# Performance work log

Hardware: AMD Instinct MI355X
Metric: run time of the kernel (lower is better)

Reference implementation:

```python
import jax, jax.numpy as jnp
import numpy as np

B, L, N, C = 16, 96, 1024, 3
EMB, GRAP, OUT, NLAYER = 64, 16, 12, 2


def setup_inputs() -> dict:
    key = jax.random.key(0)
    ks = jax.random.split(key, 16)
    s = 0.1
    return {
        "history_data": jax.random.normal(ks[0], (B, L, N, C), jnp.float32),
        # row-stochastic graph (normalized adjacency buffer)
        "adj": jax.nn.softmax(jax.random.normal(ks[1], (N, N), jnp.float32), axis=-1),
        "Wv0": jax.random.normal(ks[2], (C, EMB), jnp.float32) * s,
        "Wv1": jax.random.normal(ks[3], (EMB, EMB), jnp.float32) * s,
        "bv": jnp.zeros((NLAYER, EMB), jnp.float32),
        "E": jax.random.normal(ks[4], (NLAYER, N, EMB), jnp.float32) * s,
        "Wq": jax.random.normal(ks[5], (NLAYER, EMB, EMB), jnp.float32) * s,
        "Wk": jax.random.normal(ks[6], (NLAYER, EMB, EMB), jnp.float32) * s,
        "Eg1": jax.random.normal(ks[7], (NLAYER, N, GRAP), jnp.float32) * s,
        "Eg2": jax.random.normal(ks[8], (NLAYER, N, GRAP), jnp.float32) * s,
        "Wmix": jax.random.normal(ks[9], (NLAYER, 3, EMB, EMB), jnp.float32) * s,
        "bmix": jnp.zeros((NLAYER, EMB), jnp.float32),
        "Wgates": jax.random.normal(ks[10], (NLAYER, 4, EMB, EMB), jnp.float32) * s,
        "bgates": jnp.zeros((NLAYER, 4, EMB), jnp.float32),
        "Wdec": jax.random.normal(ks[11], (OUT, NLAYER, EMB), jnp.float32) * s,
        "bdec": jnp.zeros((OUT,), jnp.float32),
        "Wout": jax.random.normal(ks[12], (OUT, OUT), jnp.float32) * s,
        "bout": jnp.zeros((OUT,), jnp.float32),
    }


def reference(history_data, adj, Wv0, Wv1, bv, E, Wq, Wk, Eg1, Eg2,
              Wmix, bmix, Wgates, bgates, Wdec, bdec, Wout, bout):
    # GinAR forward (inference: dropout = identity, lay_norm unused in original forward).
    emb = Wv1.shape[0]
    inv = 1.0 / jnp.sqrt(jnp.float32(emb))
    x = history_data  # (B, L, N, in)
    finals = []
    for z in range(Wmix.shape[0]):
        Wv = Wv0 if z == 0 else Wv1
        # interpolation attention over variables (nodes), shared across time/batch
        q = E[z] @ Wq[z]
        k = E[z] @ Wk[z]
        attn = jax.nn.softmax((q @ k.T) * inv, axis=-1)                 # (N, N)
        # adaptive learned graph
        adp = jax.nn.softmax(jax.nn.relu(Eg1[z] @ Eg2[z].T), axis=-1)    # (N, N)
        bz, Wm, bm, Wg, bgz = bv[z], Wmix[z], bmix[z], Wgates[z], bgates[z]

        def step(ct, xt, Wv=Wv, attn=attn, adp=adp, bz=bz, Wm=Wm, bm=bm, Wg=Wg, bgz=bgz):
            v = xt @ Wv + bz                                # (B, N, emb)
            h = jnp.einsum('mn,bne->bme', attn, v)          # variable interpolation
            hg = (jnp.einsum('mn,bne->bme', adj, h) @ Wm[0]
                  + jnp.einsum('mn,bne->bme', adp, h) @ Wm[1]
                  + h @ Wm[2] + bm)                         # adaptive graph conv
            gates = jnp.einsum('bne,kef->kbnf', hg, Wg) + bgz[:, None, None, :]
            f = jax.nn.sigmoid(gates[0])
            i = jax.nn.sigmoid(gates[1])
            g = jnp.tanh(gates[2])
            o = jax.nn.sigmoid(gates[3])
            ct = f * ct + i * g
            ht = o * jnp.tanh(ct)
            return ct, ht

        ct0 = jnp.zeros((x.shape[0], x.shape[2], emb), x.dtype)
        _, hts = jax.lax.scan(step, ct0, jnp.moveaxis(x, 1, 0))  # (L, B, N, emb)
        x = jnp.moveaxis(hts, 0, 1)                              # (B, L, N, emb)
        finals.append(x[:, -1])                                  # last step -> (B, N, emb)
    final = jnp.stack(finals, axis=1)                            # (B, layers, N, emb)
    # decoder Conv2d(layer_num -> out_len, kernel (1, emb)) == contraction over (layer, emb)
    dec = jnp.einsum('blne,ole->bon', final, Wdec) + bdec[None, :, None]
    # 1x1 output conv
    out = jnp.einsum('bpn,op->bon', dec, Wout) + bout[None, :, None]
    return out  # (B, out_len, N)
```

## Files before the change

### kernel.cpp

```cpp
#include <hip/hip_runtime.h>
#include <hip/hip_bf16.h>

#define B_ 16
#define L_ 96
#define N_ 1024
#define EMB_ 64

typedef __hip_bfloat16 bf16;
typedef __attribute__((ext_vector_type(4))) float f32x4;
typedef __attribute__((ext_vector_type(8))) short s16x8;

template <int MODE>
__global__ __launch_bounds__(256) void gemm_nn(
    const float* __restrict__ A, const float* __restrict__ Bm, float* __restrict__ C,
    int M, int N, int K, int lda, int ldb, int ldc, const float* __restrict__ bias)
{
    if (MODE == 1) {
        const int bz = blockIdx.z, z = bz >> 1;
        A += (size_t)z * 65536;
        const float* Wsel = (bz & 1) ? (const float*)bias : Bm;
        Bm = Wsel + z * 4096;
        C += (size_t)bz * 65536;
        bias = nullptr;
    }
    __shared__ float As[64][17];
    __shared__ __align__(16) float Bs[16][64];
    const int tid = threadIdx.x;
    const int tx = tid & 15, ty = tid >> 4;
    const int row0 = blockIdx.y * 64, col0 = blockIdx.x * 64;
    float acc[4][4] = {};
    const int ak = tid & 15, ar = tid >> 4;
    const int bc = tid & 63, bk = tid >> 6;
    for (int k0 = 0; k0 < K; k0 += 16) {
#pragma unroll
        for (int i = 0; i < 4; ++i) {
            int r = ar + i * 16;
            int gr = row0 + r, gk = k0 + ak;
            As[r][ak] = (gr < M && gk < K) ? A[(size_t)gr * lda + gk] : 0.f;
        }
#pragma unroll
        for (int i = 0; i < 4; ++i) {
            int kk = bk + i * 4;
            int gk = k0 + kk, gc = col0 + bc;
            Bs[kk][bc] = (gk < K && gc < N) ? Bm[(size_t)gk * ldb + gc] : 0.f;
        }
        __syncthreads();
#pragma unroll
        for (int kk = 0; kk < 16; ++kk) {
            float4 b4 = *reinterpret_cast<const float4*>(&Bs[kk][tx * 4]);
            float a0 = As[ty * 4 + 0][kk];
            float a1 = As[ty * 4 + 1][kk];
            float a2 = As[ty * 4 + 2][kk];
            float a3 = As[ty * 4 + 3][kk];
            acc[0][0] += a0 * b4.x; acc[0][1] += a0 * b4.y; acc[0][2] += a0 * b4.z; acc[0][3] += a0 * b4.w;
            acc[1][0] += a1 * b4.x; acc[1][1] += a1 * b4.y; acc[1][2] += a1 * b4.z; acc[1][3] += a1 * b4.w;
            acc[2][0] += a2 * b4.x; acc[2][1] += a2 * b4.y; acc[2][2] += a2 * b4.z; acc[2][3] += a2 * b4.w;
            acc[3][0] += a3 * b4.x; acc[3][1] += a3 * b4.y; acc[3][2] += a3 * b4.z; acc[3][3] += a3 * b4.w;
        }
        __syncthreads();
    }
#pragma unroll
    for (int i = 0; i < 4; ++i) {
        int gr = row0 + ty * 4 + i;
        if (gr >= M) continue;
#pragma unroll
        for (int j = 0; j < 4; ++j) {
            int gc = col0 + tx * 4 + j;
            if (gc >= N) continue;
            float v = acc[i][j];
            if (bias) v += bias[gc];
            C[(size_t)gr * ldc + gc] = v;
        }
    }
}

__global__ __launch_bounds__(256) void gemm_nt(
    const float* __restrict__ A, const float* __restrict__ Bm, float* __restrict__ C,
    int N, int K, float alpha, int zsA, int zsB, int zsC)
{
    const int z = blockIdx.z;
    A += (size_t)z * zsA; Bm += (size_t)z * zsB; C += (size_t)z * zsC;
    __shared__ float As[64][65];
    __shared__ float Bs[64][65];
    const int tid = threadIdx.x;
    const int row0 = blockIdx.y * 64, col0 = blockIdx.x * 64;
    for (int idx = tid; idx < 64 * K; idx += 256) {
        int r = idx / K, c = idx % K;
        As[r][c] = A[(size_t)(row0 + r) * K + c];
        Bs[r][c] = Bm[(size_t)(col0 + r) * K + c];
    }
    __syncthreads();
    const int tx = tid & 15, ty = tid >> 4;
    float acc[4][4] = {};
    for (int c = 0; c < K; ++c) {
        float a[4], b[4];
#pragma unroll
        for (int i = 0; i < 4; ++i) a[i] = As[ty * 4 + i][c];
#pragma unroll
        for (int j = 0; j < 4; ++j) b[j] = Bs[tx * 4 + j][c];
#pragma unroll
        for (int i = 0; i < 4; ++i)
#pragma unroll
            for (int j = 0; j < 4; ++j) acc[i][j] += a[i] * b[j];
    }
#pragma unroll
    for (int i = 0; i < 4; ++i)
#pragma unroll
        for (int j = 0; j < 4; ++j)
            C[(size_t)(row0 + ty * 4 + i) * N + col0 + tx * 4 + j] = alpha * acc[i][j];
}

__global__ __launch_bounds__(256) void row_softmax(
    const float* __restrict__ in, float* __restrict__ out32, int os32,
    bf16* __restrict__ out16, int os16, int zs_in, int zs16, int relu)
{
    const int z = blockIdx.y;
    const float* rp = in + (size_t)z * zs_in + (size_t)blockIdx.x * N_;
    if (out32) out32 += (size_t)z * zs_in;
    if (out16) out16 += (size_t)z * zs16;
    const int tid = threadIdx.x;
    float v[4];
#pragma unroll
    for (int j = 0; j < 4; ++j) {
        float x = rp[tid + 256 * j];
        if (relu) x = fmaxf(x, 0.f);
        v[j] = x;
    }
    float m = fmaxf(fmaxf(v[0], v[1]), fmaxf(v[2], v[3]));
#pragma unroll
    for (int off = 32; off > 0; off >>= 1) m = fmaxf(m, __shfl_xor(m, off));
    __shared__ float red[4], red2[4];
    int w = tid >> 6;
    if ((tid & 63) == 0) red[w] = m;
    __syncthreads();
    m = fmaxf(fmaxf(red[0], red[1]), fmaxf(red[2], red[3]));
    float s = 0.f;
#pragma unroll
    for (int j = 0; j < 4; ++j) { v[j] = __expf(v[j] - m); s += v[j]; }
#pragma unroll
    for (int off = 32; off > 0; off >>= 1) s += __shfl_xor(s, off);
    if ((tid & 63) == 0) red2[w] = s;
    __syncthreads();
    s = red2[0] + red2[1] + red2[2] + red2[3];
    float inv = 1.f / s;
#pragma unroll
    for (int j = 0; j < 4; ++j) {
        float r = v[j] * inv;
        if (out32) out32[(size_t)blockIdx.x * os32 + tid + 256 * j] = r;
        if (out16) out16[(size_t)blockIdx.x * os16 + tid + 256 * j] = __float2bfloat16(r);
    }
}

__global__ __launch_bounds__(256) void transpose_f2b(
    const float* __restrict__ in, bf16* __restrict__ out)
{
    const int z = blockIdx.z;
    in += (size_t)z * 1048576; out += (size_t)z * 1048576;
    __shared__ float t[64][65];
    const int cx = blockIdx.x, cy = blockIdx.y;
    const int tid = threadIdx.x;
#pragma unroll
    for (int k = 0; k < 16; ++k) {
        int idx = k * 256 + tid;
        int r = idx >> 6, c = idx & 63;
        t[r][c] = in[(size_t)(cy * 64 + r) * 1024 + cx * 64 + c];
    }
    __syncthreads();
#pragma unroll
    for (int k = 0; k < 16; ++k) {
        int idx = k * 256 + tid;
        int r = idx >> 6, c = idx & 63;
        out[(size_t)(cx * 64 + r) * 1024 + cy * 64 + c] = __float2bfloat16(t[c][r]);
    }
}

__global__ __launch_bounds__(256) void wgct_kernel(const float* __restrict__ Wg,
                                                   bf16* __restrict__ WgcT)
{
    int i = blockIdx.x * 256 + threadIdx.x;
    int g = i >> 12, e = (i >> 6) & 63, f = i & 63;
    WgcT[(((size_t)g * 64 + f) << 6) + e] = __float2bfloat16(Wg[i]);
}

__global__ __launch_bounds__(256) void wvc1t_kernel(const float* __restrict__ Wvc1,
                                                    bf16* __restrict__ WT)
{
    int i = blockIdx.x * 256 + threadIdx.x;
    int row = i >> 6, f = i & 63;
    float v = 0.f;
    if (row < 192) { int kp = row >> 6, e = row & 63; v = Wvc1[kp * 4096 + f * 64 + e]; }
    WT[i] = __float2bfloat16(v);
}

__global__ __launch_bounds__(256) void f2b_kernel(const float* __restrict__ in,
                                                  bf16* __restrict__ out, int n)
{
    int i = blockIdx.x * 256 + threadIdx.x;
    if (i < n) out[i] = __float2bfloat16(in[i]);
}

__global__ __launch_bounds__(256) void bias_kernel(
    const float* __restrict__ bvz, const float* __restrict__ Wmz, const float* __restrict__ bmz,
    const float* __restrict__ Wgz, const float* __restrict__ bgz, float* __restrict__ bgconst)
{
    __shared__ float bconst[64];
    const int tid = threadIdx.x;
    if (tid < 64) {
        float s = bmz[tid];
        for (int kp = 0; kp < 3; ++kp)
            for (int f = 0; f < 64; ++f) s += bvz[f] * Wmz[kp * 4096 + f * 64 + tid];
        bconst[tid] = s;
    }
    __syncthreads();
    int g = tid >> 6, fo = tid & 63;
    float s = bgz[g * 64 + fo];
    for (int e = 0; e < 64; ++e) s += bconst[e] * Wgz[g * 4096 + e * 64 + fo];
    bgconst[tid] = s;
}

__global__ __launch_bounds__(256) void wbig_kernel(
    const float* __restrict__ Wvc0, const float* __restrict__ Wg0, bf16* __restrict__ WbigT)
{
    const int tid = threadIdx.x;
    const int g = tid >> 6, fo = tid & 63;
    float v[9];
#pragma unroll
    for (int q = 0; q < 9; ++q) {
        const int kp = q / 3, c = q % 3;
        float s = 0.f;
        for (int e = 0; e < 64; ++e)
            s += Wvc0[kp * 192 + c * 64 + e] * Wg0[g * 4096 + e * 64 + fo];
        v[q] = s;
    }
#pragma unroll
    for (int i = 0; i < 32; ++i)
        WbigT[(size_t)tid * 32 + i] = __float2bfloat16(i < 9 ? v[i] : 0.f);
}

__global__ __launch_bounds__(256) void xt_build(
    const float* __restrict__ hist, bf16* __restrict__ XT)
{
    __shared__ float xs[3][1024];
    const int lb = blockIdx.x;
    const int l = lb >> 4, b = lb & 15;
    const int tid = threadIdx.x;
    const float* xp = hist + ((size_t)b * L_ + l) * N_ * 3;
    for (int i = tid; i < 3072; i += 256) xs[i % 3][i / 3] = xp[i];
    __syncthreads();
#pragma unroll
    for (int c = 0; c < 3; ++c)
#pragma unroll
        for (int q = 0; q < 4; ++q) {
            int n = q * 256 + tid;
            XT[((size_t)lb * 3 + c) * 1024 + n] = __float2bfloat16(xs[c][n]);
        }
}

__device__ __forceinline__ void gload16(const bf16* g, bf16* l)
{
    __builtin_amdgcn_global_load_lds((const __attribute__((address_space(1))) void*)g,
                                     (__attribute__((address_space(3))) void*)l, 16, 0, 0);
}

template <int OUT_BF16, int REMAP>
__global__ __launch_bounds__(256) void gemm_mfma(
    const bf16* __restrict__ A, const bf16* __restrict__ BT, void* __restrict__ Cp,
    int M, int N, int K, int lda, int ldb, int ldc,
    const float* __restrict__ bias, int Nmask)
{
    __shared__ __align__(16) bf16 As[128 * 64];
    __shared__ __align__(16) bf16 Bs[128 * 64];
    const int tid = threadIdx.x;
    const int lane = tid & 63, w = tid >> 6;
    const int wr = w >> 1, wc = w & 1;
    const int row0 = blockIdx.y * 128, col0 = blockIdx.x * 128;
    if (REMAP == 1) BT += (size_t)blockIdx.z * 64;
    if (REMAP == 2) A += (size_t)blockIdx.z * 1024;
    if (REMAP == 3) {
        const int z3 = blockIdx.z >> 1, wh = blockIdx.z & 1;
        if (wh) A = BT + (size_t)z3 * 1048576;
        BT = (const bf16*)bias + (size_t)z3 * 1048576;
        Cp = (void*)((bf16*)Cp + (size_t)z3 * 3145728 + (size_t)wh * 1024);
        bias = nullptr;
    }

    f32x4 acc[4][4];
#pragma unroll
    for (int i = 0; i < 4; ++i)
#pragma unroll
        for (int j = 0; j < 4; ++j) acc[i][j] = (f32x4){0.f, 0.f, 0.f, 0.f};

    const int srow = w * 32 + (lane >> 3);
    const int scolsw = ((lane & 7) ^ (lane >> 3)) * 8;

    for (int k0 = 0; k0 < K; k0 += 64) {
#pragma unroll
        for (int i = 0; i < 4; ++i) {
            gload16(A + (size_t)(row0 + srow + i * 8) * lda + k0 + scolsw,
                    &As[(w * 32 + i * 8) * 64]);
            gload16(BT + (size_t)(col0 + srow + i * 8) * ldb + k0 + scolsw,
                    &Bs[(w * 32 + i * 8) * 64]);
        }
        __syncthreads();
#pragma unroll
        for (int kk = 0; kk < 64; kk += 32) {
            s16x8 af[4], bfr[4];
            const int ko = (kk + (lane >> 4) * 8) ^ ((lane & 7) << 3);
#pragma unroll
            for (int mi = 0; mi < 4; ++mi)
                af[mi] = *(const s16x8*)&As[(wr * 64 + mi * 16 + (lane & 15)) * 64 + ko];
#pragma unroll
            for (int ni = 0; ni < 4; ++ni)
                bfr[ni] = *(const s16x8*)&Bs[(wc * 64 + ni * 16 + (lane & 15)) * 64 + ko];
#pragma unroll
            for (int mi = 0; mi < 4; ++mi)
#pragma unroll
                for (int ni = 0; ni < 4; ++ni)
                    acc[mi][ni] = __builtin_amdgcn_mfma_f32_16x16x32_bf16(
                        af[mi], bfr[ni], acc[mi][ni], 0, 0, 0);
        }
        __syncthreads();
    }

    if (REMAP == 1) {
        bf16* outb = (bf16*)Cp + (size_t)blockIdx.z * (64 * 3072);
#pragma unroll
        for (int mi = 0; mi < 4; ++mi) {
            const int gr = row0 + wr * 64 + mi * 16 + (lane >> 4) * 4;
#pragma unroll
            for (int ni = 0; ni < 4; ++ni) {
                const int gc = col0 + wc * 64 + ni * 16 + (lane & 15);
#pragma unroll
                for (int j = 0; j < 4; ++j) {
                    const int r = gr + j;
                    if (r >= Nmask) continue;
                    outb[(size_t)(r & 63) * 3072 + (r >> 6) * 1024 + gc] =
                        __float2bfloat16(acc[mi][ni][j]);
                }
            }
        }
        return;
    }
    if (REMAP == 2) {
        bf16* outb = (bf16*)Cp;
        const int kpoff = blockIdx.z * 3;
#pragma unroll
        for (int mi = 0; mi < 4; ++mi) {
            const int gr = row0 + wr * 64 + mi * 16 + (lane >> 4) * 4;
#pragma unroll
            for (int ni = 0; ni < 4; ++ni) {
                const int gc = col0 + wc * 64 + ni * 16 + (lane & 15);
                if (gc >= Nmask) continue;
                const int dstc = (gc / 3) * 32 + kpoff + gc % 3;
#pragma unroll
                for (int j = 0; j < 4; ++j)
                    outb[(size_t)(gr + j) * ldc + dstc] = __float2bfloat16(acc[mi][ni][j]);
            }
        }
        return;
    }

#pragma unroll
    for (int mi = 0; mi < 4; ++mi) {
        const int gr = row0 + wr * 64 + mi * 16 + (lane >> 4) * 4;
#pragma unroll
        for (int ni = 0; ni < 4; ++ni) {
            const int gc = col0 + wc * 64 + ni * 16 + (lane & 15);
            if (gc >= Nmask) continue;
            const float bb = bias ? bias[gc] : 0.f;
#pragma unroll
            for (int j = 0; j < 4; ++j) {
                float v = acc[mi][ni][j] + bb;
                if (OUT_BF16)
                    ((bf16*)Cp)[(size_t)(gr + j) * ldc + gc] = __float2bfloat16(v);
                else
                    ((float*)Cp)[(size_t)(gr + j) * ldc + gc] = v;
            }
        }
    }
}

__global__ __launch_bounds__(512) void gemm_pipe(
    const bf16* __restrict__ A, const bf16* __restrict__ BT, bf16* __restrict__ C,
    int N, int K)
{
    __shared__ __align__(16) bf16 lds[8 * 8192];
    const int tid = threadIdx.x;
    const int lane = tid & 63, w = tid >> 6;
    const int wm = w >> 2, wn = w & 3, bh = wn >> 1;
    const int row0 = blockIdx.y * 256, col0 = blockIdx.x * 256;

    const int strow = tid >> 3;
    const int srck  = ((tid & 7) ^ ((tid >> 3) & 7)) << 3;
    const int e7 = lane & 7, fs = lane >> 4, a15 = lane & 15;

    int aoff0[8], boff0[4];
#pragma unroll
    for (int mi = 0; mi < 8; ++mi)
        aoff0[mi] = (mi * 16 + a15) * 64 + ((fs ^ e7) << 3);
#pragma unroll
    for (int ni = 0; ni < 4; ++ni)
        boff0[ni] = ((wn & 1) * 64 + ni * 16 + a15) * 64 + ((fs ^ e7) << 3);

    auto stage = [&](int mat, int half, int kt) {
        bf16* dst = &lds[(size_t)((((kt & 1) << 1) | mat) * 2 + half) * 8192 + w * 512];
        const bf16* src = (mat ? BT + (size_t)col0 * K : A + (size_t)row0 * K)
                          + (size_t)(half * 128) * K + kt * 64 + srck;
        gload16(src + (size_t)strow * K, dst);
        gload16(src + (size_t)(64 + strow) * K, dst + 4096);
    };

    f32x4 acc[8][4];
#pragma unroll
    for (int i = 0; i < 8; ++i)
#pragma unroll
        for (int j = 0; j < 4; ++j) acc[i][j] = (f32x4){0.f, 0.f, 0.f, 0.f};

    s16x8 b0, b1, b2, b3;

#define MF_(a, mi) { \
    acc[mi][0] = __builtin_amdgcn_mfma_f32_16x16x32_bf16(a, b0, acc[mi][0], 0, 0, 0); \
    acc[mi][1] = __builtin_amdgcn_mfma_f32_16x16x32_bf16(a, b1, acc[mi][1], 0, 0, 0); \
    acc[mi][2] = __builtin_amdgcn_mfma_f32_16x16x32_bf16(a, b2, acc[mi][2], 0, 0, 0); \
    acc[mi][3] = __builtin_amdgcn_mfma_f32_16x16x32_bf16(a, b3, acc[mi][3], 0, 0, 0); }

#define PH_(d, kh, g, DOB, STG) { \
    const bf16* Ab = &lds[((d) * 4 + wm) * 8192]; \
    const bf16* Bb = &lds[((d) * 4 + 2 + bh) * 8192]; \
    if (DOB) { \
        b0 = *(const s16x8*)&Bb[boff0[0] ^ ((kh) * 32)]; \
        b1 = *(const s16x8*)&Bb[boff0[1] ^ ((kh) * 32)]; \
        b2 = *(const s16x8*)&Bb[boff0[2] ^ ((kh) * 32)]; \
        b3 = *(const s16x8*)&Bb[boff0[3] ^ ((kh) * 32)]; \
    } \
    s16x8 a0 = *(const s16x8*)&Ab[aoff0[(g) * 4 + 0] ^ ((kh) * 32)]; \
    s16x8 a1 = *(const s16x8*)&Ab[aoff0[(g) * 4 + 1] ^ ((kh) * 32)]; \
    s16x8 a2 = *(const s16x8*)&Ab[aoff0[(g) * 4 + 2] ^ ((kh) * 32)]; \
    s16x8 a3 = *(const s16x8*)&Ab[aoff0[(g) * 4 + 3] ^ ((kh) * 32)]; \
    STG; \
    __builtin_amdgcn_s_barrier(); \
    asm volatile("s_waitcnt lgkmcnt(0)" ::: "memory"); \
    __builtin_amdgcn_sched_barrier(0); \
    __builtin_amdgcn_s_setprio(1); \
    MF_(a0, (g) * 4 + 0); MF_(a1, (g) * 4 + 1); \
    MF_(a2, (g) * 4 + 2); MF_(a3, (g) * 4 + 3); \
    __builtin_amdgcn_s_setprio(0); \
    __builtin_amdgcn_s_barrier(); }

    const int NT = K >> 6;
    stage(0, 0, 0); stage(0, 1, 0); stage(1, 0, 0); stage(1, 1, 0);
    stage(0, 0, 1);

    for (int i = 0; i < NT / 2; ++i) {
        const int kt = 2 * i;
        asm volatile("s_waitcnt vmcnt(2)" ::: "memory");
        __builtin_amdgcn_sched_barrier(0);
        __builtin_amdgcn_s_barrier();
        PH_(0, 0, 0, 1, { stage(0, 1, kt + 1); });
        PH_(0, 0, 1, 0, { stage(1, 0, kt + 1); });
        PH_(0, 1, 0, 1, { stage(1, 1, kt + 1); });
        PH_(0, 1, 1, 0, { if (kt + 2 < NT) stage(0, 0, kt + 2); });
        if (kt + 2 < NT) { asm volatile("s_waitcnt vmcnt(2)" ::: "memory"); }
        else             { asm volatile("s_waitcnt vmcnt(0)" ::: "memory"); }
        __builtin_amdgcn_sched_barrier(0);
        __builtin_amdgcn_s_barrier();
        PH_(1, 0, 0, 1, { if (kt + 2 < NT) stage(0, 1, kt + 2); });
        PH_(1, 0, 1, 0, { if (kt + 2 < NT) stage(1, 0, kt + 2); });
        PH_(1, 1, 0, 1, { if (kt + 2 < NT) stage(1, 1, kt + 2); });
        PH_(1, 1, 1, 0, { if (kt + 3 < NT) stage(0, 0, kt + 3); });
    }
#undef PH_
#undef MF_

#pragma unroll
    for (int mi = 0; mi < 8; ++mi) {
        const int gr = row0 + wm * 128 + mi * 16 + (lane >> 4) * 4;
#pragma unroll
        for (int ni = 0; ni < 4; ++ni) {
            const int gc = col0 + wn * 64 + ni * 16 + (lane & 15);
#pragma unroll
            for (int j = 0; j < 4; ++j)
                C[(size_t)(gr + j) * N + gc] = __float2bfloat16(acc[mi][ni][j]);
        }
    }
}

__global__ __launch_bounds__(256, 4) void fused_gates_scan(
    const bf16* __restrict__ HG, const bf16* __restrict__ WgcT,
    const float* __restrict__ bgc, float* __restrict__ ct_buf,
    bf16* __restrict__ ht_out, float* __restrict__ htlast,
    int LC, int l0, int initct)
{
    __shared__ __align__(16) bf16 Bs[256 * 64];
    __shared__ float bgs[256];
    const int tid = threadIdx.x;
    const int lane = tid & 63, w = tid >> 6;
    const int n = blockIdx.x;
    const int swz = ((lane & 7) ^ (lane >> 3)) * 8;
    const int l8 = (lane >> 3) * 64;

#pragma unroll
    for (int r = 0; r < 8; ++r)
        gload16(WgcT + r * 2048 + w * 512 + l8 + swz, &Bs[r * 2048 + w * 512]);
    bgs[tid] = bgc[tid];
    __syncthreads();

    const int ar = lane & 15;
    const int ak = (lane >> 4) * 8;
    const int kswz = (lane & 7) << 3;
    const int f = w * 16 + ar;
    const int r0 = (lane >> 4) * 4;
    const float bgf = bgs[f], bgi = bgs[64 + f], bgg = bgs[128 + f], bgo = bgs[192 + f];

    float ct[4];
    const size_t cbase = (size_t)n * 1024;
#pragma unroll
    for (int j = 0; j < 4; ++j)
        ct[j] = initct ? 0.f : ct_buf[cbase + (size_t)(r0 + j) * 64 + f];

    const bf16* HGn = HG + (size_t)n * LC * 1024;
    s16x8 a0 = *(const s16x8*)&HGn[ar * 64 + ak];
    s16x8 a1 = *(const s16x8*)&HGn[ar * 64 + ak + 32];

    for (int l = 0; l < LC; ++l) {
        s16x8 p0 = a0, p1 = a1;
        if (l + 1 < LC) {
            p0 = *(const s16x8*)&HGn[((l + 1) * 16 + ar) * 64 + ak];
            p1 = *(const s16x8*)&HGn[((l + 1) * 16 + ar) * 64 + ak + 32];
        }
        f32x4 acc[4];
#pragma unroll
        for (int ni = 0; ni < 4; ++ni) acc[ni] = (f32x4){0.f, 0.f, 0.f, 0.f};
#pragma unroll
        for (int ni = 0; ni < 4; ++ni) {
            s16x8 bf = *(const s16x8*)&Bs[(ni * 64 + w * 16 + ar) * 64 + (ak ^ kswz)];
            acc[ni] = __builtin_amdgcn_mfma_f32_16x16x32_bf16(a0, bf, acc[ni], 0, 0, 0);
        }
#pragma unroll
        for (int ni = 0; ni < 4; ++ni) {
            s16x8 bf = *(const s16x8*)&Bs[(ni * 64 + w * 16 + ar) * 64 + ((ak + 32) ^ kswz)];
            acc[ni] = __builtin_amdgcn_mfma_f32_16x16x32_bf16(a1, bf, acc[ni], 0, 0, 0);
        }
        const size_t hbase = ((size_t)n * LC + l) * 1024;
        const bool last = (l0 + l == L_ - 1);
#pragma unroll
        for (int j = 0; j < 4; ++j) {
            float xf = acc[0][j] + bgf;
            float xi = acc[1][j] + bgi;
            float xg = acc[2][j] + bgg;
            float xo = acc[3][j] + bgo;
            float fg = 1.f / (1.f + __expf(-xf));
            float ig = 1.f / (1.f + __expf(-xi));
            float gg = 2.f / (1.f + __expf(-2.f * xg)) - 1.f;
            float og = 1.f / (1.f + __expf(-xo));
            ct[j] = fg * ct[j] + ig * gg;
            float ht = og * (2.f / (1.f + __expf(-2.f * ct[j])) - 1.f);
            if (ht_out) ht_out[hbase + (size_t)(r0 + j) * 64 + f] = __float2bfloat16(ht);
            if (htlast && last) htlast[cbase + (size_t)(r0 + j) * 64 + f] = ht;
        }
        a0 = p0; a1 = p1;
    }
#pragma unroll
    for (int j = 0; j < 4; ++j)
        ct_buf[cbase + (size_t)(r0 + j) * 64 + f] = ct[j];
}

__global__ __launch_bounds__(256, 4) void fused_gates_scan_y(
    const bf16* __restrict__ Y, const bf16* __restrict__ WbigT,
    const float* __restrict__ bgc, float* __restrict__ ct_buf,
    bf16* __restrict__ ht_out, float* __restrict__ htlast,
    int LC, int l0, int initct)
{
    __shared__ bf16 Bs2[256 * 40];
    __shared__ float bgs[256];
    const int tid = threadIdx.x;
    const int lane = tid & 63, w = tid >> 6;
    const int n = blockIdx.x;
    {
        const uint4* src = (const uint4*)(WbigT + (size_t)tid * 32);
        uint4* dst = (uint4*)&Bs2[tid * 40];
        dst[0] = src[0]; dst[1] = src[1]; dst[2] = src[2]; dst[3] = src[3];
    }
    bgs[tid] = bgc[tid];
    __syncthreads();

    const int ar = lane & 15, fs = lane >> 4;
    const int f = w * 16 + ar;
    const int r0 = fs * 4;
    const float bgf = bgs[f], bgi = bgs[64 + f], bgg = bgs[128 + f], bgo = bgs[192 + f];

    float ct[4];
    const size_t cbase = (size_t)n * 1024;
#pragma unroll
    for (int j = 0; j < 4; ++j)
        ct[j] = initct ? 0.f : ct_buf[cbase + (size_t)(r0 + j) * 64 + f];

    const bf16* Yn = Y + (size_t)n * LC * 512;
    s16x8 a = *(const s16x8*)&Yn[ar * 32 + fs * 8];

    for (int l = 0; l < LC; ++l) {
        s16x8 p = a;
        if (l + 1 < LC) p = *(const s16x8*)&Yn[((l + 1) * 16 + ar) * 32 + fs * 8];
        f32x4 acc[4];
#pragma unroll
        for (int ni = 0; ni < 4; ++ni) {
            s16x8 bf = *(const s16x8*)&Bs2[(ni * 64 + w * 16 + ar) * 40 + fs * 8];
            acc[ni] = __builtin_amdgcn_mfma_f32_16x16x32_bf16(
                a, bf, (f32x4){0.f, 0.f, 0.f, 0.f}, 0, 0, 0);
        }
        const size_t hbase = ((size_t)n * LC + l) * 1024;
        const bool last = (l0 + l == L_ - 1);
#pragma unroll
        for (int j = 0; j < 4; ++j) {
            float xf = acc[0][j] + bgf;
            float xi = acc[1][j] + bgi;
            float xg = acc[2][j] + bgg;
            float xo = acc[3][j] + bgo;
            float fg = 1.f / (1.f + __expf(-xf));
            float ig = 1.f / (1.f + __expf(-xi));
            float gg = 2.f / (1.f + __expf(-2.f * xg)) - 1.f;
            float og = 1.f / (1.f + __expf(-xo));
            ct[j] = fg * ct[j] + ig * gg;
            float ht = og * (2.f / (1.f + __expf(-2.f * ct[j])) - 1.f);
            if (ht_out) ht_out[hbase + (size_t)(r0 + j) * 64 + f] = __float2bfloat16(ht);
            if (htlast && last) htlast[cbase + (size_t)(r0 + j) * 64 + f] = ht;
        }
        a = p;
    }
#pragma unroll
    for (int j = 0; j < 4; ++j)
        ct_buf[cbase + (size_t)(r0 + j) * 64 + f] = ct[j];
}

__global__ __launch_bounds__(256) void decoder_kernel(
    const float* __restrict__ h0, const float* __restrict__ h1,
    const float* __restrict__ Wdec, const float* __restrict__ bdec,
    const float* __restrict__ Wout, const float* __restrict__ bout,
    float* __restrict__ outp)
{
    __shared__ float Wd[12 * 2 * 64];
    __shared__ float Wo[144];
    __shared__ float bd[12], bo[12];
    const int tid = threadIdx.x;
    for (int i = tid; i < 12 * 2 * 64; i += 256) Wd[i] = Wdec[i];
    for (int i = tid; i < 144; i += 256) Wo[i] = Wout[i];
    if (tid < 12) { bd[tid] = bdec[tid]; bo[tid] = bout[tid]; }
    __syncthreads();
    const int gid = blockIdx.x * 256 + tid;
    const int b = gid >> 10, n = gid & 1023;
    const float* h0r = h0 + ((size_t)n * 16 + b) * 64;
    const float* h1r = h1 + ((size_t)n * 16 + b) * 64;
    float dec[12];
#pragma unroll
    for (int o = 0; o < 12; ++o) dec[o] = bd[o];
    for (int e = 0; e < 64; ++e) {
        float v0 = h0r[e], v1 = h1r[e];
#pragma unroll
        for (int o = 0; o < 12; ++o) dec[o] += v0 * Wd[o * 128 + e] + v1 * Wd[o * 128 + 64 + e];
    }
#pragma unroll
    for (int o = 0; o < 12; ++o) {
        float s = bo[o];
#pragma unroll
        for (int p = 0; p < 12; ++p) s += Wo[o * 12 + p] * dec[p];
        outp[((size_t)b * 12 + o) * 1024 + n] = s;
    }
}

extern "C" void kernel_launch(void* const* d_in, const int* in_sizes, int n_in,
                              void* d_out, int out_size, void* d_ws, size_t ws_size,
                              hipStream_t stream)
{
    const float* hist = (const float*)d_in[0];
    const float* adj  = (const float*)d_in[1];
    const float* Wv0  = (const float*)d_in[2];
    const float* Wv1  = (const float*)d_in[3];
    const float* bv   = (const float*)d_in[4];
    const float* E    = (const float*)d_in[5];
    const float* Wq   = (const float*)d_in[6];
    const float* Wk   = (const float*)d_in[7];
    const float* Eg1  = (const float*)d_in[8];
    const float* Eg2  = (const float*)d_in[9];
    const float* Wmix = (const float*)d_in[10];
    const float* bmix = (const float*)d_in[11];
    const float* Wg   = (const float*)d_in[12];
    const float* bg   = (const float*)d_in[13];
    const float* Wdec = (const float*)d_in[14];
    const float* bdec = (const float*)d_in[15];
    const float* Wout = (const float*)d_in[16];
    const float* bout = (const float*)d_in[17];
    float* outp = (float*)d_out;
    (void)in_sizes; (void)n_in; (void)out_size;

    char* ws = (char*)d_ws;
    size_t off = 0;
    auto alloc = [&](size_t bytes) -> void* {
        void* p = (void*)(ws + off);
        off += (bytes + 255) & ~(size_t)255;
        return p;
    };
    bf16*  Mcatb  = (bf16*)alloc((size_t)2 * 1024 * 3072 * 2);
    bf16*  attnT2 = (bf16*)alloc((size_t)2 * 1024 * 1024 * 2);
    bf16*  adjb   = (bf16*)alloc((size_t)1024 * 1024 * 2);
    bf16*  adpb2  = (bf16*)alloc((size_t)2 * 1024 * 1024 * 2);
    float* qkb    = (float*)alloc((size_t)4 * 1024 * 64 * 4);
    float* logit2 = (float*)alloc((size_t)2 * 1024 * 1024 * 4);
    float* Wvc0   = (float*)alloc(3 * 3 * 64 * 4);
    float* Wvc1   = (float*)alloc(3 * 64 * 64 * 4);
    bf16*  Wvc1T  = (bf16*)alloc(256 * 64 * 2);
    bf16*  WgcT1  = (bf16*)alloc(256 * 64 * 2);
    bf16*  WbigT  = (bf16*)alloc(256 * 32 * 2);
    float* bgc0   = (float*)alloc(256 * 4);
    float* bgc1   = (float*)alloc(256 * 4);
    float* ct0    = (float*)alloc((size_t)N_ * B_ * 64 * 4);
    float* ct1    = (float*)alloc((size_t)N_ * B_ * 64 * 4);
    float* hl0    = (float*)alloc((size_t)N_ * B_ * 64 * 4);
    float* hl1    = (float*)alloc((size_t)N_ * B_ * 64 * 4);
    bf16*  XT     = (bf16*)alloc((size_t)L_ * 16 * 3 * 1024 * 2);
    size_t fixed = off;

    static const int divs[] = {16, 8};
    int LC = 8;
    for (int di = 0; di < 2; ++di) {
        if (fixed + (size_t)divs[di] * 9437184ull + 65536 <= ws_size) { LC = divs[di]; break; }
    }
    bf16*  VcatT = (bf16*)alloc((size_t)LC * 6291456ull);
    bf16*  HGht  = (bf16*)alloc((size_t)LC * 2097152ull);
    bf16*  Y     = (bf16*)alloc((size_t)LC * 1048576ull);

    dim3 blk(256);
    bf16*  McatB[2] = {Mcatb, Mcatb + 3145728};
    float* bgc[2] = {bgc0, bgc1};

    f2b_kernel<<<4096, blk, 0, stream>>>(adj, adjb, 1024 * 1024);
    gemm_nn<1><<<dim3(1, 16, 4), blk, 0, stream>>>(E, Wq, qkb,
        1024, 64, 64, 64, 64, 64, (const float*)Wk);
    gemm_nt<<<dim3(16, 16, 2), blk, 0, stream>>>(qkb, qkb + 65536, logit2,
        1024, 64, 0.125f, 131072, 131072, 1048576);
    row_softmax<<<dim3(1024, 2), blk, 0, stream>>>(logit2, logit2, 1024,
        Mcatb + 2048, 3072, 1048576, 3145728, 0);
    transpose_f2b<<<dim3(16, 16, 2), blk, 0, stream>>>(logit2, attnT2);
    gemm_nt<<<dim3(16, 16, 2), blk, 0, stream>>>(Eg1, Eg2, logit2,
        1024, 16, 1.f, 16384, 16384, 1048576);
    row_softmax<<<dim3(1024, 2), blk, 0, stream>>>(logit2, nullptr, 0,
        adpb2, 1024, 1048576, 1048576, 1);
    for (int kp = 0; kp < 3; ++kp)
        gemm_nn<0><<<dim3(1, 1), blk, 0, stream>>>(Wv0, Wmix + kp * 4096,
            Wvc0 + kp * 3 * 64, 3, 64, 64, 64, 64, 64, nullptr);
    wbig_kernel<<<1, blk, 0, stream>>>(Wvc0, Wg, WbigT);
    for (int kp = 0; kp < 3; ++kp)
        gemm_nn<0><<<dim3(1, 1), blk, 0, stream>>>(Wv1, Wmix + 12288 + kp * 4096,
            Wvc1 + kp * 4096, 64, 64, 64, 64, 64, 64, nullptr);
    wvc1t_kernel<<<64, blk, 0, stream>>>(Wvc1, Wvc1T);
    wgct_kernel<<<64, blk, 0, stream>>>(Wg + 16384, WgcT1);
    bias_kernel<<<1, blk, 0, stream>>>(bv, Wmix, bmix, Wg, bg, bgc0);
    bias_kernel<<<1, blk, 0, stream>>>(bv + 64, Wmix + 12288, bmix + 64,
        Wg + 16384, bg + 256, bgc1);
    gemm_mfma<1, 3><<<dim3(8, 8, 4), blk, 0, stream>>>(adjb, adpb2, Mcatb,
        1024, 1024, 1024, 1024, 1024, 3072, (const float*)attnT2, 1024);

    hipMemsetAsync(Y, 0, (size_t)LC * 1048576ull, stream);
    xt_build<<<L_ * 16, blk, 0, stream>>>(hist, XT);

    const int nch = L_ / LC;
    dim3 blk512(512);
    for (int c = 0; c < nch; ++c) {
        const int l0 = c * LC;
        gemm_mfma<1, 2><<<dim3(LC * 48 / 128, 8, 3), blk, 0, stream>>>(McatB[0],
            XT + (size_t)l0 * 49152, Y,
            1024, LC * 48, 1024, 3072, 1024, LC * 512, nullptr, LC * 48);
        fused_gates_scan_y<<<1024, blk, 0, stream>>>(Y, WbigT, bgc0, ct0,
            HGht, hl0, LC, l0, c == 0);
        gemm_mfma<1, 1><<<dim3(8, 2, LC * 16), blk, 0, stream>>>(Wvc1T, HGht, VcatT,
            256, 1024, 64, 64, LC * 1024, 0, nullptr, 192);
        gemm_pipe<<<dim3(LC * 4, 4), blk512, 0, stream>>>(McatB[1], VcatT, HGht,
            LC * 1024, 3072);
        fused_gates_scan<<<1024, blk, 0, stream>>>(HGht, WgcT1, bgc1, ct1,
            nullptr, hl1, LC, l0, c == 0);
    }
    decoder_kernel<<<64, blk, 0, stream>>>(hl0, hl1, Wdec, bdec, Wout, bout, outp);
}
```

Baseline: 1.570 ms.

## Batch layer-0 work over the whole sequence and defer layer-1 scan when workspace allows

```diff
diff --git a/kernel.cpp b/kernel.cpp
--- a/kernel.cpp
+++ b/kernel.cpp
@@ -382,7 +382,7 @@
 
 __global__ __launch_bounds__(512) void gemm_pipe(
     const bf16* __restrict__ A, const bf16* __restrict__ BT, bf16* __restrict__ C,
-    int N, int K)
+    int Nc, int K)
 {
     __shared__ __align__(16) bf16 lds[8 * 8192];
     const int tid = threadIdx.x;
@@ -480,7 +480,7 @@
             const int gc = col0 + wn * 64 + ni * 16 + (lane & 15);
 #pragma unroll
             for (int j = 0; j < 4; ++j)
-                C[(size_t)(gr + j) * N + gc] = __float2bfloat16(acc[mi][ni][j]);
+                C[(size_t)(gr + j) * Nc + gc] = __float2bfloat16(acc[mi][ni][j]);
         }
     }
 }
@@ -719,18 +719,36 @@
     bf16*  XT     = (bf16*)alloc((size_t)L_ * 16 * 3 * 1024 * 2);
     size_t fixed = off;
 
-    static const int divs[] = {16, 8};
-    int LC = 8;
-    for (int di = 0; di < 2; ++di) {
-        if (fixed + (size_t)divs[di] * 9437184ull + 65536 <= ws_size) { LC = divs[di]; break; }
-    }
-    bf16*  VcatT = (bf16*)alloc((size_t)LC * 6291456ull);
-    bf16*  HGht  = (bf16*)alloc((size_t)LC * 2097152ull);
-    bf16*  Y     = (bf16*)alloc((size_t)LC * 1048576ull);
+    const size_t YALL_B = (size_t)1024 * L_ * 16 * 32 * 2;
+    const size_t HT_B   = (size_t)1024 * L_ * 16 * 64 * 2;
+    const size_t GUARD  = 1 << 20;
+    int plan;  int LC;
+    if (fixed + YALL_B + HT_B + (size_t)16 * 6291456ull + HT_B + GUARD <= ws_size) {
+        plan = 0; LC = 16;
+    } else if (fixed + YALL_B + HT_B + (size_t)16 * 6291456ull
+               + (size_t)16 * 2097152ull + GUARD <= ws_size) {
+        plan = 1; LC = 16;
+    } else if (fixed + (size_t)16 * 9437184ull + GUARD <= ws_size) {
+        plan = 2; LC = 16;
+    } else {
+        plan = 2; LC = 8;
+    }
+
+    bf16 *Yall = nullptr, *ht0 = nullptr, *VcatT = nullptr, *HG = nullptr, *Ychunk = nullptr;
+    if (plan <= 1) {
+        Yall  = (bf16*)alloc(YALL_B);
+        ht0   = (bf16*)alloc(HT_B);
+        VcatT = (bf16*)alloc((size_t)LC * 6291456ull);
+        HG    = (bf16*)alloc(plan == 0 ? HT_B : (size_t)LC * 2097152ull);
+    } else {
+        VcatT  = (bf16*)alloc((size_t)LC * 6291456ull);
+        HG     = (bf16*)alloc((size_t)LC * 2097152ull);
+        Ychunk = (bf16*)alloc((size_t)LC * 1048576ull);
+    }
 
     dim3 blk(256);
+    dim3 blk512(512);
     bf16*  McatB[2] = {Mcatb, Mcatb + 3145728};
-    float* bgc[2] = {bgc0, bgc1};
 
     f2b_kernel<<<4096, blk, 0, stream>>>(adj, adjb, 1024 * 1024);
     gemm_nn<1><<<dim3(1, 16, 4), blk, 0, stream>>>(E, Wq, qkb,
@@ -759,24 +777,50 @@
     gemm_mfma<1, 3><<<dim3(8, 8, 4), blk, 0, stream>>>(adjb, adpb2, Mcatb,
         1024, 1024, 1024, 1024, 1024, 3072, (const float*)attnT2, 1024);
 
-    hipMemsetAsync(Y, 0, (size_t)LC * 1048576ull, stream);
     xt_build<<<L_ * 16, blk, 0, stream>>>(hist, XT);
 
-    const int nch = L_ / LC;
-    dim3 blk512(512);
-    for (int c = 0; c < nch; ++c) {
-        const int l0 = c * LC;
-        gemm_mfma<1, 2><<<dim3(LC * 48 / 128, 8, 3), blk, 0, stream>>>(McatB[0],
-            XT + (size_t)l0 * 49152, Y,
-            1024, LC * 48, 1024, 3072, 1024, LC * 512, nullptr, LC * 48);
-        fused_gates_scan_y<<<1024, blk, 0, stream>>>(Y, WbigT, bgc0, ct0,
-            HGht, hl0, LC, l0, c == 0);
-        gemm_mfma<1, 1><<<dim3(8, 2, LC * 16), blk, 0, stream>>>(Wvc1T, HGht, VcatT,
-            256, 1024, 64, 64, LC * 1024, 0, nullptr, 192);
-        gemm_pipe<<<dim3(LC * 4, 4), blk512, 0, stream>>>(McatB[1], VcatT, HGht,
-            LC * 1024, 3072);
-        fused_gates_scan<<<1024, blk, 0, stream>>>(HGht, WgcT1, bgc1, ct1,
-            nullptr, hl1, LC, l0, c == 0);
+    if (plan <= 1) {
+        hipMemsetAsync(Yall, 0, YALL_B, stream);
+        gemm_mfma<1, 2><<<dim3(L_ * 48 / 128, 8, 3), blk, 0, stream>>>(McatB[0],
+            XT, Yall, 1024, L_ * 48, 1024, 3072, 1024, L_ * 512, nullptr, L_ * 48);
+        fused_gates_scan_y<<<1024, blk, 0, stream>>>(Yall, WbigT, bgc0, ct0,
+            ht0, hl0, L_, 0, 1);
+        const int nch = L_ / LC;
+        for (int c = 0; c < nch; ++c) {
+            const int l0 = c * LC;
+            gemm_mfma<1, 1><<<dim3(8, 2, LC * 16), blk, 0, stream>>>(Wvc1T,
+                ht0 + (size_t)l0 * 1024, VcatT,
+                256, 1024, 64, 64, L_ * 1024, 0, nullptr, 192);
+            if (plan == 0) {
+                gemm_pipe<<<dim3(LC * 4, 4), blk512, 0, stream>>>(McatB[1], VcatT,
+                    HG + (size_t)l0 * 1024, L_ * 1024, 3072);
+            } else {
+                gemm_pipe<<<dim3(LC * 4, 4), blk512, 0, stream>>>(McatB[1], VcatT,
+                    HG, LC * 1024, 3072);
+                fused_gates_scan<<<1024, blk, 0, stream>>>(HG, WgcT1, bgc1, ct1,
+                    nullptr, hl1, LC, l0, c == 0);
+            }
+        }
+        if (plan == 0)
+            fused_gates_scan<<<1024, blk, 0, stream>>>(HG, WgcT1, bgc1, ct1,
+                nullptr, hl1, L_, 0, 1);
+    } else {
+        hipMemsetAsync(Ychunk, 0, (size_t)LC * 1048576ull, stream);
+        const int nch = L_ / LC;
+        for (int c = 0; c < nch; ++c) {
+            const int l0 = c * LC;
+            gemm_mfma<1, 2><<<dim3(LC * 48 / 128, 8, 3), blk, 0, stream>>>(McatB[0],
+                XT + (size_t)l0 * 49152, Ychunk,
+                1024, LC * 48, 1024, 3072, 1024, LC * 512, nullptr, LC * 48);
+            fused_gates_scan_y<<<1024, blk, 0, stream>>>(Ychunk, WbigT, bgc0, ct0,
+                HG, hl0, LC, l0, c == 0);
+            gemm_mfma<1, 1><<<dim3(8, 2, LC * 16), blk, 0, stream>>>(Wvc1T, HG, VcatT,
+                256, 1024, 64, 64, LC * 1024, 0, nullptr, 192);
+            gemm_pipe<<<dim3(LC * 4, 4), blk512, 0, stream>>>(McatB[1], VcatT, HG,
+                LC * 1024, 3072);
+            fused_gates_scan<<<1024, blk, 0, stream>>>(HG, WgcT1, bgc1, ct1,
+                nullptr, hl1, LC, l0, c == 0);
+        }
     }
     decoder_kernel<<<64, blk, 0, stream>>>(hl0, hl1, Wdec, bdec, Wout, bout, outp);
 }
```

New measurement: 1.588 ms. About the same (+1.1%).
